# Optimization experiments

Hardware: AMD Instinct MI355X
Metric: run time of the kernel (lower is better)

## Reference

```python
import jax, jax.numpy as jnp
import numpy as np

B, T, D, F, E = 2, 2048, 1024, 4096, 8
TOP_K = 2


def setup_inputs() -> dict:
    key = jax.random.key(0)
    k0, k1, k2, k3 = jax.random.split(key, 4)
    x = jax.random.normal(k0, (B, T, D), dtype=jnp.float32)
    Wr = jax.random.normal(k1, (D, E), dtype=jnp.float32) * 0.02   # router (no bias)
    W1 = jax.random.normal(k2, (E, D, F), dtype=jnp.float32) * 0.02
    b1 = jnp.zeros((E, F), dtype=jnp.float32)
    W2 = jax.random.normal(k3, (E, F, D), dtype=jnp.float32) * 0.02
    b2 = jnp.zeros((E, D), dtype=jnp.float32)
    return {"x": x, "Wr": Wr, "W1": W1, "b1": b1, "W2": W2, "b2": b2}


def reference(x, Wr, W1, b1, W2, b2):
    # Router: softmax over experts, top-k select, renormalize selected probs.
    logits = jnp.einsum('btd,de->bte', x, Wr)                      # [B,T,E]
    probs = jax.nn.softmax(logits, axis=-1)
    top_v, top_i = jax.lax.top_k(probs, TOP_K)                     # [B,T,K]
    top_v = top_v / jnp.sum(top_v, axis=-1, keepdims=True)
    # Combine weights: scatter renormalized top-k probs back to expert slots.
    combine = jnp.sum(jax.nn.one_hot(top_i, E, dtype=x.dtype) * top_v[..., None], axis=-2)  # [B,T,E]
    # Expert FFNs (Linear -> exact GELU -> Linear); dropout inactive at eval.
    h = jax.nn.gelu(jnp.einsum('btd,edf->ebtf', x, W1) + b1[:, None, None, :],
                    approximate=False)                              # [E,B,T,F]
    y = jnp.einsum('ebtf,efd->ebtd', h, W2) + b2[:, None, None, :]  # [E,B,T,D]
    # Weighted sum over selected experts (combine is zero for unselected).
    out = jnp.einsum('ebtd,bte->btd', y, combine)
    return out
```

## Files before the change

### kernel.cpp

```cpp
#include <hip/hip_runtime.h>
#include <hip/hip_bf16.h>
#include <math.h>

#define B_  2
#define T_  2048
#define D_  1024
#define F_  4096
#define E_  8
#define NTOK 4096
#define TOPK 2
#define NROW 8192

typedef unsigned short bf16_t;
typedef float f32x4 __attribute__((ext_vector_type(4)));
typedef int   i32x4 __attribute__((ext_vector_type(4)));
typedef __bf16 bf16x8 __attribute__((ext_vector_type(8)));

#define OFF_CNT   0
#define OFF_BASE  32
#define OFF_TIDX  64
#define OFF_TW    32832
#define OFF_LIST  65600
#define OFF_WGT   196672
#define OFF_H_OLD 327744
#define WS_OLD    (OFF_H_OLD + (size_t)NROW * F_ * 2)
#define OFF_SLOT  327744
#define OFF_XB    (1u << 20)
#define OFF_W1T   (OFF_XB  + (size_t)NTOK * D_ * 2)
#define OFF_W2T   (OFF_W1T + (size_t)E_ * F_ * D_ * 2)
#define OFF_HN    (OFF_W2T + (size_t)E_ * D_ * F_ * 2)
#define OFF_Y     (OFF_HN  + (size_t)NROW * F_ * 2)
#define WS_MFMA   (OFF_Y + (size_t)NROW * D_ * 4)
#define WS_MFMA2  (OFF_Y + 2 * (size_t)NROW * D_ * 4)

__device__ __forceinline__ float gelu_exact(float v) {
    return 0.5f * v * (1.0f + erff(v * 0.70710678118654752440f));
}

__device__ __forceinline__ unsigned short f2bf_rne(float f) {
    union { float f; unsigned int u; } v; v.f = f;
    unsigned int r = (v.u + 0x7fffu + ((v.u >> 16) & 1u)) >> 16;
    return (unsigned short)r;
}

__device__ __forceinline__ float bf2f(unsigned int u) {
    union { unsigned int i; float f; } v; v.i = u << 16; return v.f;
}

__device__ __forceinline__ void gld16(const void* g, void* l) {
    __builtin_amdgcn_global_load_lds(
        (const __attribute__((address_space(1))) unsigned int*)g,
        (__attribute__((address_space(3))) unsigned int*)l, 16, 0, 0);
}

__device__ __forceinline__ void mfma16(const i32x4& a, const i32x4& b, f32x4& c) {
    c = __builtin_amdgcn_mfma_f32_16x16x32_bf16(
        __builtin_bit_cast(bf16x8, a), __builtin_bit_cast(bf16x8, b), c, 0, 0, 0);
}

__global__ __launch_bounds__(64) void router_kernel(
    const float* __restrict__ x, const float* __restrict__ Wr,
    int* __restrict__ top_idx, float* __restrict__ top_w,
    int* __restrict__ cnt, int* __restrict__ list, float* __restrict__ wgt,
    int* __restrict__ slot, int mode)
{
    const int n = blockIdx.x;
    const int lane = threadIdx.x;
    const float* xr = x + (size_t)n * D_;

    float acc[E_];
#pragma unroll
    for (int e = 0; e < E_; ++e) acc[e] = 0.f;

    for (int d = lane; d < D_; d += 64) {
        const float xv = xr[d];
#pragma unroll
        for (int e = 0; e < E_; ++e)
            acc[e] += xv * Wr[d * E_ + e];
    }
#pragma unroll
    for (int e = 0; e < E_; ++e) {
        float v = acc[e];
#pragma unroll
        for (int off = 32; off > 0; off >>= 1)
            v += __shfl_down(v, off, 64);
        acc[e] = v;
    }
    if (lane == 0) {
        float m = acc[0];
#pragma unroll
        for (int e = 1; e < E_; ++e) m = fmaxf(m, acc[e]);
        float p[E_];
#pragma unroll
        for (int e = 0; e < E_; ++e) p[e] = __expf(acc[e] - m);
        int i0 = 0; float v0 = p[0];
#pragma unroll
        for (int e = 1; e < E_; ++e) if (p[e] > v0) { v0 = p[e]; i0 = e; }
        int i1 = (i0 == 0) ? 1 : 0; float v1 = p[i1];
#pragma unroll
        for (int e = 0; e < E_; ++e) {
            if (e == i0) continue;
            if (p[e] > v1) { v1 = p[e]; i1 = e; }
        }
        const float inv = 1.f / (v0 + v1);
        const float w0 = v0 * inv, w1 = v1 * inv;
        top_idx[n * TOPK + 0] = i0;
        top_idx[n * TOPK + 1] = i1;
        top_w[n * TOPK + 0] = w0;
        top_w[n * TOPK + 1] = w1;
        if (mode & 1) {
            int p0 = atomicAdd(&cnt[i0], 1);
            list[i0 * NTOK + p0] = n;  wgt[i0 * NTOK + p0] = w0;
            int p1 = atomicAdd(&cnt[i1], 1);
            list[i1 * NTOK + p1] = n;  wgt[i1 * NTOK + p1] = w1;
            if (mode & 2) {
                slot[n * TOPK + 0] = (i0 << 16) | p0;
                slot[n * TOPK + 1] = (i1 << 16) | p1;
            }
        }
    }
}

__global__ void prefix_kernel(const int* __restrict__ cnt, int* __restrict__ base)
{
    if (threadIdx.x == 0 && blockIdx.x == 0) {
        int s = 0;
#pragma unroll
        for (int e = 0; e < E_; ++e) { base[e] = s; s += cnt[e]; }
    }
}

__global__ __launch_bounds__(256) void convert_x_kernel(
    const float* __restrict__ x, bf16_t* __restrict__ xb)
{
    const int i = blockIdx.x * 256 + threadIdx.x;
    const float4 v = ((const float4*)x)[i];
    uint2 o;
    o.x = (unsigned int)f2bf_rne(v.x) | ((unsigned int)f2bf_rne(v.y) << 16);
    o.y = (unsigned int)f2bf_rne(v.z) | ((unsigned int)f2bf_rne(v.w) << 16);
    ((uint2*)xb)[i] = o;
}

__global__ __launch_bounds__(256) void transpose_kernel(
    const float* __restrict__ src, bf16_t* __restrict__ dst, int R, int C)
{
    __shared__ float tile[64][65];
    const int z  = blockIdx.z;
    const int r0 = blockIdx.y * 64;
    const int c0 = blockIdx.x * 64;
    const float* s = src + (size_t)z * R * C;
    bf16_t*      d = dst + (size_t)z * R * C;
#pragma unroll
    for (int i = 0; i < 4; ++i) {
        const int r  = i * 16 + (threadIdx.x >> 4);
        const int c4 = (threadIdx.x & 15) * 4;
        const float4 v = *(const float4*)(s + (size_t)(r0 + r) * C + c0 + c4);
        tile[r][c4]     = v.x;
        tile[r][c4 + 1] = v.y;
        tile[r][c4 + 2] = v.z;
        tile[r][c4 + 3] = v.w;
    }
    __syncthreads();
    const int rc = (threadIdx.x & 15) * 4;
    const int cc = threadIdx.x >> 4;
#pragma unroll
    for (int i = 0; i < 4; ++i) {
        const int c = i * 16 + cc;
        uint2 o;
        o.x = (unsigned int)f2bf_rne(tile[rc    ][c]) | ((unsigned int)f2bf_rne(tile[rc + 1][c]) << 16);
        o.y = (unsigned int)f2bf_rne(tile[rc + 2][c]) | ((unsigned int)f2bf_rne(tile[rc + 3][c]) << 16);
        *(uint2*)(d + (size_t)(c0 + c) * R + r0 + rc) = o;
    }
}

template<int G>
__global__ __launch_bounds__(512, 2) void mg8_kernel(
    const bf16_t* __restrict__ Amat, const bf16_t* __restrict__ Bmat,
    const float* __restrict__ bias,
    const int* __restrict__ cnt, const int* __restrict__ base,
    const int* __restrict__ list,
    bf16_t* __restrict__ Hout, float* __restrict__ Yout)
{
    __shared__ __align__(16) bf16_t sm[3 * 16384];

    const int e  = (G == 1) ? blockIdx.z : (blockIdx.z % E_);
    const int ce = cnt[e];
    const int m0 = blockIdx.y * 256;
    if (m0 >= ce) return;
    const int n0 = blockIdx.x * 256;
    const int be = base[e];

    const int Kfull = (G == 1) ? D_ : F_;
    int klen, kbase, slab;
    if (G == 1) { klen = D_; kbase = 0; slab = 0; }
    else {
        const int kslabs = gridDim.z / E_;
        slab  = blockIdx.z / E_;
        klen  = F_ / kslabs;
        kbase = slab * klen;
    }
    const int nk = klen / 32;

    const int tid  = threadIdx.x;
    const int lane = tid & 63, wave = tid >> 6;
    const int l16 = lane & 15, quad = lane >> 4;
    const int wm = wave >> 2, wn = wave & 3;

    const int srow = wave * 16 + (lane >> 2);
    const int sgc  = (lane & 3) ^ ((srow >> 1) & 3);
    int rA0 = m0 + srow;        if (rA0 >= ce) rA0 = ce - 1;
    int rA1 = m0 + srow + 128;  if (rA1 >= ce) rA1 = ce - 1;
    const bf16_t *gA0, *gA1;
    if (G == 1) {
        gA0 = Amat + (size_t)list[e * NTOK + rA0] * D_ + sgc * 8;
        gA1 = Amat + (size_t)list[e * NTOK + rA1] * D_ + sgc * 8;
    } else {
        gA0 = Amat + (size_t)(be + rA0) * F_ + kbase + sgc * 8;
        gA1 = Amat + (size_t)(be + rA1) * F_ + kbase + sgc * 8;
    }
    const bf16_t* Be  = Bmat + (size_t)e * F_ * D_;
    const bf16_t* gB0 = Be + (size_t)(n0 + srow) * Kfull + kbase + sgc * 8;
    const bf16_t* gB1 = Be + (size_t)(n0 + srow + 128) * Kfull + kbase + sgc * 8;

#define STG(bb, kk) do { \
        bf16_t* la = sm + (bb) * 16384 + wave * 512; \
        bf16_t* lb = la + 8192; \
        gld16(gA0 + (kk), la); \
        gld16(gA1 + (kk), la + 4096); \
        gld16(gB0 + (kk), lb); \
        gld16(gB1 + (kk), lb + 4096); } while (0)

    const int swz  = (quad ^ ((l16 >> 1) & 3)) * 8;
    const int aoff = (wm * 128 + l16) * 32 + swz;
    const int boff = 8192 + (wn * 64 + l16) * 32 + swz;

    f32x4 acc[8][4] = {};

    STG(0, 0);
    STG(1, 32);
    asm volatile("s_waitcnt vmcnt(4)" ::: "memory");
    __builtin_amdgcn_s_barrier();
    __builtin_amdgcn_sched_barrier(0);

    int rb = 0;
    for (int t = 0; t < nk; ++t) {
        if (t + 2 < nk) {
            int wb = rb + 2; if (wb >= 3) wb -= 3;
            STG(wb, (t + 2) * 32);
        }
        const bf16_t* bp = sm + rb * 16384;
        i32x4 af[8], bv[4];
#pragma unroll
        for (int m = 0; m < 8; ++m)
            af[m] = *(const i32x4*)(bp + aoff + m * 512);
#pragma unroll
        for (int n = 0; n < 4; ++n)
            bv[n] = *(const i32x4*)(bp + boff + n * 512);
        __builtin_amdgcn_s_setprio(1);
#pragma unroll
        for (int m = 0; m < 8; ++m)
#pragma unroll
            for (int n = 0; n < 4; ++n)
                mfma16(af[m], bv[n], acc[m][n]);
        __builtin_amdgcn_s_setprio(0);
        if (t + 1 < nk) {
            if (t + 2 < nk) asm volatile("s_waitcnt vmcnt(4)" ::: "memory");
            else            asm volatile("s_waitcnt vmcnt(0)" ::: "memory");
            __builtin_amdgcn_s_barrier();
            __builtin_amdgcn_sched_barrier(0);
        }
        rb = (rb == 2) ? 0 : rb + 1;
    }
#undef STG

    if (G == 1) {
        const float* b1e = bias + (size_t)e * F_;
#pragma unroll
        for (int n = 0; n < 4; ++n) {
            const int col = n0 + wn * 64 + n * 16 + l16;
            const float bb = b1e[col];
#pragma unroll
            for (int m = 0; m < 8; ++m) {
                const int pr = m0 + wm * 128 + m * 16 + quad * 4;
#pragma unroll
                for (int r = 0; r < 4; ++r) {
                    const int p = pr + r;
                    if (p < ce)
                        Hout[(size_t)(be + p) * F_ + col] =
                            f2bf_rne(gelu_exact(acc[m][n][r] + bb));
                }
            }
        }
    } else {
        float* Ys = Yout + (size_t)slab * NROW * D_;
        const float* b2e = bias + (size_t)e * D_;
#pragma unroll
        for (int n = 0; n < 4; ++n) {
            const int col = n0 + wn * 64 + n * 16 + l16;
            const float bb = (slab == 0) ? b2e[col] : 0.f;
#pragma unroll
            for (int m = 0; m < 8; ++m) {
                const int pr = m0 + wm * 128 + m * 16 + quad * 4;
#pragma unroll
                for (int r = 0; r < 4; ++r) {
                    const int p = pr + r;
                    if (p < ce)
                        Ys[(size_t)(be + p) * D_ + col] = acc[m][n][r] + bb;
                }
            }
        }
    }
}

__global__ __launch_bounds__(256) void combine_kernel(
    const float* __restrict__ Y, const int* __restrict__ slot,
    const float* __restrict__ tw, const int* __restrict__ base,
    float* __restrict__ out, int kslabs)
{
    const int n = blockIdx.x;
    const int t = threadIdx.x;
    const int s0 = slot[n * TOPK + 0], s1 = slot[n * TOPK + 1];
    const float w0 = tw[n * TOPK + 0], w1 = tw[n * TOPK + 1];
    const int r0 = base[s0 >> 16] + (s0 & 0xffff);
    const int r1 = base[s1 >> 16] + (s1 & 0xffff);
    float4 y0 = ((const float4*)(Y + (size_t)r0 * D_))[t];
    float4 y1 = ((const float4*)(Y + (size_t)r1 * D_))[t];
    if (kslabs == 2) {
        const float* Y1 = Y + (size_t)NROW * D_;
        const float4 a = ((const float4*)(Y1 + (size_t)r0 * D_))[t];
        const float4 b = ((const float4*)(Y1 + (size_t)r1 * D_))[t];
        y0.x += a.x; y0.y += a.y; y0.z += a.z; y0.w += a.w;
        y1.x += b.x; y1.y += b.y; y1.z += b.z; y1.w += b.w;
    }
    float4 o;
    o.x = w0 * y0.x + w1 * y1.x;
    o.y = w0 * y0.y + w1 * y1.y;
    o.z = w0 * y0.z + w1 * y1.z;
    o.w = w0 * y0.w + w1 * y1.w;
    ((float4*)(out + (size_t)n * D_))[t] = o;
}

#define BM 128
#define BN 128
#define BK 16

__global__ __launch_bounds__(256) void gemm1_kernel(
    const float* __restrict__ x, const float* __restrict__ W1,
    const float* __restrict__ b1,
    const int* __restrict__ cnt, const int* __restrict__ base,
    const int* __restrict__ list, bf16_t* __restrict__ H)
{
    __shared__ __align__(16) float Xs[BK][BM + 4];
    __shared__ __align__(16) float Ws[BK][BN + 4];

    const int e  = blockIdx.z;
    const int ce = cnt[e];
    const int m0 = blockIdx.y * BM;
    if (m0 >= ce) return;
    const int n0 = blockIdx.x * BN;
    const int be = base[e];
    const int t  = threadIdx.x;
    const int tx = t & 15, ty = t >> 4;

    const int xr_row = t >> 1;
    const int xr_c0  = (t & 1) * 8;
    const int p_x    = m0 + xr_row;
    const float* xrow = (p_x < ce) ? (x + (size_t)list[e * NTOK + p_x] * D_) : nullptr;
    const int wr_kk = t >> 4;
    const int wr_c0 = (t & 15) * 8;
    const float* W1e = W1 + (size_t)e * D_ * F_;

    float acc[8][8];
#pragma unroll
    for (int i = 0; i < 8; ++i)
#pragma unroll
        for (int j = 0; j < 8; ++j) acc[i][j] = 0.f;

    for (int k0 = 0; k0 < D_; k0 += BK) {
        float xv[8];
        if (xrow) {
            const float4 a = *(const float4*)(xrow + k0 + xr_c0);
            const float4 b = *(const float4*)(xrow + k0 + xr_c0 + 4);
            xv[0]=a.x; xv[1]=a.y; xv[2]=a.z; xv[3]=a.w;
            xv[4]=b.x; xv[5]=b.y; xv[6]=b.z; xv[7]=b.w;
        } else {
#pragma unroll
            for (int j = 0; j < 8; ++j) xv[j] = 0.f;
        }
#pragma unroll
        for (int j = 0; j < 8; ++j) Xs[xr_c0 + j][xr_row] = xv[j];
        {
            const float* wr = W1e + (size_t)(k0 + wr_kk) * F_ + (n0 + wr_c0);
            *(float4*)&Ws[wr_kk][wr_c0]     = *(const float4*)(wr);
            *(float4*)&Ws[wr_kk][wr_c0 + 4] = *(const float4*)(wr + 4);
        }
        __syncthreads();
#pragma unroll 4
        for (int kk = 0; kk < BK; ++kk) {
            float a[8], b[8];
            *(float4*)&a[0] = *(const float4*)&Xs[kk][ty * 8];
            *(float4*)&a[4] = *(const float4*)&Xs[kk][ty * 8 + 4];
            *(float4*)&b[0] = *(const float4*)&Ws[kk][tx * 8];
            *(float4*)&b[4] = *(const float4*)&Ws[kk][tx * 8 + 4];
#pragma unroll
            for (int i = 0; i < 8; ++i)
#pragma unroll
                for (int j = 0; j < 8; ++j)
                    acc[i][j] += a[i] * b[j];
        }
        __syncthreads();
    }

    const float* b1e = b1 + (size_t)e * F_;
    float bb[8];
#pragma unroll
    for (int j = 0; j < 8; ++j) bb[j] = b1e[n0 + tx * 8 + j];
#pragma unroll
    for (int i = 0; i < 8; ++i) {
        const int p = m0 + ty * 8 + i;
        if (p >= ce) continue;
        unsigned int pk[4];
#pragma unroll
        for (int jj = 0; jj < 4; ++jj) {
            const float g0 = gelu_exact(acc[i][2 * jj]     + bb[2 * jj]);
            const float g1 = gelu_exact(acc[i][2 * jj + 1] + bb[2 * jj + 1]);
            pk[jj] = (unsigned int)f2bf_rne(g0) | ((unsigned int)f2bf_rne(g1) << 16);
        }
        uint4 v; v.x = pk[0]; v.y = pk[1]; v.z = pk[2]; v.w = pk[3];
        *(uint4*)(H + (size_t)(be + p) * F_ + n0 + tx * 8) = v;
    }
}

__global__ __launch_bounds__(256) void gemm2_kernel(
    const bf16_t* __restrict__ H, const float* __restrict__ W2,
    const float* __restrict__ b2,
    const int* __restrict__ cnt, const int* __restrict__ base,
    const int* __restrict__ list, const float* __restrict__ wgt,
    float* __restrict__ out)
{
    __shared__ __align__(16) float Hs[BK][BM + 4];
    __shared__ __align__(16) float Ws[BK][BN + 4];

    const int e  = blockIdx.z;
    const int ce = cnt[e];
    const int m0 = blockIdx.y * BM;
    if (m0 >= ce) return;
    const int n0 = blockIdx.x * BN;
    const int be = base[e];
    const int t  = threadIdx.x;
    const int tx = t & 15, ty = t >> 4;

    const int hr_row = t >> 1;
    const int hr_c0  = (t & 1) * 8;
    const int p_h    = m0 + hr_row;
    const bf16_t* hrow = (p_h < ce) ? (H + (size_t)(be + p_h) * F_) : nullptr;
    const int wr_kk = t >> 4;
    const int wr_c0 = (t & 15) * 8;
    const float* W2e = W2 + (size_t)e * F_ * D_;

    float acc[8][8];
#pragma unroll
    for (int i = 0; i < 8; ++i)
#pragma unroll
        for (int j = 0; j < 8; ++j) acc[i][j] = 0.f;

    for (int k0 = 0; k0 < F_; k0 += BK) {
        float hv[8];
        if (hrow) {
            const uint4 u = *(const uint4*)(hrow + k0 + hr_c0);
            hv[0] = bf2f(u.x & 0xffffu); hv[1] = bf2f(u.x >> 16);
            hv[2] = bf2f(u.y & 0xffffu); hv[3] = bf2f(u.y >> 16);
            hv[4] = bf2f(u.z & 0xffffu); hv[5] = bf2f(u.z >> 16);
            hv[6] = bf2f(u.w & 0xffffu); hv[7] = bf2f(u.w >> 16);
        } else {
#pragma unroll
            for (int j = 0; j < 8; ++j) hv[j] = 0.f;
        }
#pragma unroll
        for (int j = 0; j < 8; ++j) Hs[hr_c0 + j][hr_row] = hv[j];
        {
            const float* wr = W2e + (size_t)(k0 + wr_kk) * D_ + (n0 + wr_c0);
            *(float4*)&Ws[wr_kk][wr_c0]     = *(const float4*)(wr);
            *(float4*)&Ws[wr_kk][wr_c0 + 4] = *(const float4*)(wr + 4);
        }
        __syncthreads();
#pragma unroll 4
        for (int kk = 0; kk < BK; ++kk) {
            float a[8], b[8];
            *(float4*)&a[0] = *(const float4*)&Hs[kk][ty * 8];
            *(float4*)&a[4] = *(const float4*)&Hs[kk][ty * 8 + 4];
            *(float4*)&b[0] = *(const float4*)&Ws[kk][tx * 8];
            *(float4*)&b[4] = *(const float4*)&Ws[kk][tx * 8 + 4];
#pragma unroll
            for (int i = 0; i < 8; ++i)
#pragma unroll
                for (int j = 0; j < 8; ++j)
                    acc[i][j] += a[i] * b[j];
        }
        __syncthreads();
    }

    const float* b2e = b2 + (size_t)e * D_;
    float bb[8];
#pragma unroll
    for (int j = 0; j < 8; ++j) bb[j] = b2e[n0 + tx * 8 + j];
#pragma unroll
    for (int i = 0; i < 8; ++i) {
        const int p = m0 + ty * 8 + i;
        if (p >= ce) continue;
        const int   n = list[e * NTOK + p];
        const float w = wgt[e * NTOK + p];
        float* op = out + (size_t)n * D_ + n0 + tx * 8;
#pragma unroll
        for (int j = 0; j < 8; ++j)
            atomicAdd(&op[j], w * (acc[i][j] + bb[j]));
    }
}

__global__ __launch_bounds__(256) void fallback_expert_kernel(
    const float* __restrict__ x,
    const float* __restrict__ W1, const float* __restrict__ b1,
    const float* __restrict__ W2, const float* __restrict__ b2,
    const int* __restrict__ top_idx, const float* __restrict__ top_w,
    float* __restrict__ out)
{
    __shared__ float x_lds[D_];
    __shared__ float h_lds[F_];

    const int n = blockIdx.x;
    const int t = threadIdx.x;

    ((float4*)x_lds)[t] = ((const float4*)(x + (size_t)n * D_))[t];
    __syncthreads();

    const int d0 = t * 4;
    float acc_out[4] = {0.f, 0.f, 0.f, 0.f};

    for (int k = 0; k < TOPK; ++k) {
        const int   e = top_idx[n * TOPK + k];
        const float w = top_w[n * TOPK + k];
        const float* W1e = W1 + (size_t)e * D_ * F_;
        const float* b1e = b1 + (size_t)e * F_;
#pragma unroll
        for (int tile = 0; tile < 2; ++tile) {
            const int base_f = tile * 2048 + t * 8;
            float a[8];
#pragma unroll
            for (int j = 0; j < 8; ++j) a[j] = b1e[base_f + j];
            const float4* wp = (const float4*)(W1e + base_f);
            for (int d = 0; d < D_; ++d) {
                const float4 w0 = wp[(size_t)d * (F_ / 4)];
                const float4 w1 = wp[(size_t)d * (F_ / 4) + 1];
                const float xv = x_lds[d];
                a[0] += xv * w0.x; a[1] += xv * w0.y;
                a[2] += xv * w0.z; a[3] += xv * w0.w;
                a[4] += xv * w1.x; a[5] += xv * w1.y;
                a[6] += xv * w1.z; a[7] += xv * w1.w;
            }
#pragma unroll
            for (int j = 0; j < 8; ++j)
                h_lds[base_f + j] = gelu_exact(a[j]);
        }
        __syncthreads();

        const float* W2e = W2 + (size_t)e * F_ * D_;
        const float* b2e = b2 + (size_t)e * D_;
        float y[4];
#pragma unroll
        for (int j = 0; j < 4; ++j) y[j] = b2e[d0 + j];
        const float4* wp2 = (const float4*)(W2e + d0);
        for (int f = 0; f < F_; ++f) {
            const float4 wv = wp2[(size_t)f * (D_ / 4)];
            const float hv = h_lds[f];
            y[0] += hv * wv.x; y[1] += hv * wv.y;
            y[2] += hv * wv.z; y[3] += hv * wv.w;
        }
#pragma unroll
        for (int j = 0; j < 4; ++j) acc_out[j] += w * y[j];
        __syncthreads();
    }

    float4 o; o.x = acc_out[0]; o.y = acc_out[1]; o.z = acc_out[2]; o.w = acc_out[3];
    *(float4*)(out + (size_t)n * D_ + d0) = o;
}

extern "C" void kernel_launch(void* const* d_in, const int* in_sizes, int n_in,
                              void* d_out, int out_size, void* d_ws, size_t ws_size,
                              hipStream_t stream) {
    const float* x  = (const float*)d_in[0];
    const float* Wr = (const float*)d_in[1];
    const float* W1 = (const float*)d_in[2];
    const float* b1 = (const float*)d_in[3];
    const float* W2 = (const float*)d_in[4];
    const float* b2 = (const float*)d_in[5];
    float* out = (float*)d_out;

    char* ws = (char*)d_ws;
    int*    cnt   = (int*)(ws + OFF_CNT);
    int*    basep = (int*)(ws + OFF_BASE);
    int*    tidx  = (int*)(ws + OFF_TIDX);
    float*  tw    = (float*)(ws + OFF_TW);
    int*    list  = (int*)(ws + OFF_LIST);
    float*  wgt   = (float*)(ws + OFF_WGT);

    if (ws_size >= WS_MFMA) {
        const int kslabs = (ws_size >= WS_MFMA2) ? 2 : 1;
        int*    slot = (int*)(ws + OFF_SLOT);
        bf16_t* Xb   = (bf16_t*)(ws + OFF_XB);
        bf16_t* W1T  = (bf16_t*)(ws + OFF_W1T);
        bf16_t* W2T  = (bf16_t*)(ws + OFF_W2T);
        bf16_t* H    = (bf16_t*)(ws + OFF_HN);
        float*  Y    = (float*)(ws + OFF_Y);

        hipMemsetAsync(cnt, 0, E_ * sizeof(int), stream);
        router_kernel<<<NTOK, 64, 0, stream>>>(x, Wr, tidx, tw, cnt, list, wgt, slot, 3);
        prefix_kernel<<<1, 64, 0, stream>>>(cnt, basep);
        convert_x_kernel<<<NTOK * D_ / 4 / 256, 256, 0, stream>>>(x, Xb);
        transpose_kernel<<<dim3(F_ / 64, D_ / 64, E_), 256, 0, stream>>>(W1, W1T, D_, F_);
        transpose_kernel<<<dim3(D_ / 64, F_ / 64, E_), 256, 0, stream>>>(W2, W2T, F_, D_);
        mg8_kernel<1><<<dim3(F_ / 256, NTOK / 256, E_), 512, 0, stream>>>(
            Xb, W1T, b1, cnt, basep, list, H, nullptr);
        mg8_kernel<2><<<dim3(D_ / 256, NTOK / 256, E_ * kslabs), 512, 0, stream>>>(
            H, W2T, b2, cnt, basep, nullptr, nullptr, Y);
        combine_kernel<<<NTOK, 256, 0, stream>>>(Y, slot, tw, basep, out, kslabs);
    } else if (ws_size >= WS_OLD) {
        bf16_t* H = (bf16_t*)(ws + OFF_H_OLD);
        hipMemsetAsync(cnt, 0, E_ * sizeof(int), stream);
        router_kernel<<<NTOK, 64, 0, stream>>>(x, Wr, tidx, tw, cnt, list, wgt, nullptr, 1);
        prefix_kernel<<<1, 64, 0, stream>>>(cnt, basep);
        hipMemsetAsync(out, 0, (size_t)NTOK * D_ * sizeof(float), stream);
        gemm1_kernel<<<dim3(F_ / BN, NTOK / BM, E_), 256, 0, stream>>>(
            x, W1, b1, cnt, basep, list, H);
        gemm2_kernel<<<dim3(D_ / BN, NTOK / BM, E_), 256, 0, stream>>>(
            H, W2, b2, cnt, basep, list, wgt, out);
    } else {
        router_kernel<<<NTOK, 64, 0, stream>>>(x, Wr, tidx, tw, cnt, list, wgt, nullptr, 0);
        fallback_expert_kernel<<<NTOK, 256, 0, stream>>>(
            x, W1, b1, W2, b2, tidx, tw, out);
    }
}
```

Baseline: 736.1 us.

## Switch grouped GEMM to BK=64 double-buffered LDS pipeline

Replaces the three-stage BK=32 LDS pipeline with a two-stage BK=64 double buffer. The swizzle changes to an 8-way XOR over 64-column rows, and each wave issues eight 16-byte global-to-LDS loads per stage. The aim is to halve the number of barriers and loop iterations per K. In exchange the prefetch distance drops from two stages to one. The kernel now waits at a full __syncthreads instead of a partial vmcnt wait, so memory latency may be less well hidden.

Measured after the change: 730.7 us. About the same (-0.7%).

```diff
diff --git a/kernel.cpp b/kernel.cpp
--- a/kernel.cpp
+++ b/kernel.cpp
@@ -181,7 +181,7 @@
     const int* __restrict__ list,
     bf16_t* __restrict__ Hout, float* __restrict__ Yout)
 {
-    __shared__ __align__(16) bf16_t sm[3 * 16384];
+    __shared__ __align__(16) bf16_t sm[2 * 32768];
 
     const int e  = (G == 1) ? blockIdx.z : (blockIdx.z % E_);
     const int ce = cnt[e];
@@ -199,77 +199,73 @@
         klen  = F_ / kslabs;
         kbase = slab * klen;
     }
-    const int nk = klen / 32;
+    const int nkt = klen / 64;
 
     const int tid  = threadIdx.x;
     const int lane = tid & 63, wave = tid >> 6;
     const int l16 = lane & 15, quad = lane >> 4;
     const int wm = wave >> 2, wn = wave & 3;
 
-    const int srow = wave * 16 + (lane >> 2);
-    const int sgc  = (lane & 3) ^ ((srow >> 1) & 3);
-    int rA0 = m0 + srow;        if (rA0 >= ce) rA0 = ce - 1;
-    int rA1 = m0 + srow + 128;  if (rA1 >= ce) rA1 = ce - 1;
-    const bf16_t *gA0, *gA1;
-    if (G == 1) {
-        gA0 = Amat + (size_t)list[e * NTOK + rA0] * D_ + sgc * 8;
-        gA1 = Amat + (size_t)list[e * NTOK + rA1] * D_ + sgc * 8;
-    } else {
-        gA0 = Amat + (size_t)(be + rA0) * F_ + kbase + sgc * 8;
-        gA1 = Amat + (size_t)(be + rA1) * F_ + kbase + sgc * 8;
-    }
-    const bf16_t* Be  = Bmat + (size_t)e * F_ * D_;
-    const bf16_t* gB0 = Be + (size_t)(n0 + srow) * Kfull + kbase + sgc * 8;
-    const bf16_t* gB1 = Be + (size_t)(n0 + srow + 128) * Kfull + kbase + sgc * 8;
-
-#define STG(bb, kk) do { \
-        bf16_t* la = sm + (bb) * 16384 + wave * 512; \
-        bf16_t* lb = la + 8192; \
-        gld16(gA0 + (kk), la); \
-        gld16(gA1 + (kk), la + 4096); \
-        gld16(gB0 + (kk), lb); \
-        gld16(gB1 + (kk), lb + 4096); } while (0)
-
-    const int swz  = (quad ^ ((l16 >> 1) & 3)) * 8;
-    const int aoff = (wm * 128 + l16) * 32 + swz;
-    const int boff = 8192 + (wn * 64 + l16) * 32 + swz;
+    const int srowl = lane >> 3;
+    const int sgc   = ((lane & 7) ^ srowl) * 8;
+
+    const bf16_t* gA[4];
+    const bf16_t* gB[4];
+    const bf16_t* Be = Bmat + (size_t)e * F_ * D_;
+#pragma unroll
+    for (int i = 0; i < 4; ++i) {
+        int ra = m0 + wave * 32 + i * 8 + srowl;
+        if (ra >= ce) ra = ce - 1;
+        if (G == 1) gA[i] = Amat + (size_t)list[e * NTOK + ra] * D_ + sgc;
+        else        gA[i] = Amat + (size_t)(be + ra) * F_ + kbase + sgc;
+        const int rb = n0 + wave * 32 + i * 8 + srowl;
+        gB[i] = Be + (size_t)rb * Kfull + kbase + sgc;
+    }
+
+#define STG(bb, koff) do { \
+        bf16_t* la = sm + (bb) * 32768 + wave * 2048; \
+        bf16_t* lb = la + 16384; \
+        gld16(gA[0] + (koff), la); \
+        gld16(gA[1] + (koff), la + 512); \
+        gld16(gA[2] + (koff), la + 1024); \
+        gld16(gA[3] + (koff), la + 1536); \
+        gld16(gB[0] + (koff), lb); \
+        gld16(gB[1] + (koff), lb + 512); \
+        gld16(gB[2] + (koff), lb + 1024); \
+        gld16(gB[3] + (koff), lb + 1536); } while (0)
+
+    const int swzk[2] = { (quad ^ (l16 & 7)) * 8, ((4 + quad) ^ (l16 & 7)) * 8 };
+    const int arow = (wm * 128 + l16) * 64;
+    const int brow = 16384 + (wn * 64 + l16) * 64;
 
     f32x4 acc[8][4] = {};
 
     STG(0, 0);
-    STG(1, 32);
-    asm volatile("s_waitcnt vmcnt(4)" ::: "memory");
-    __builtin_amdgcn_s_barrier();
-    __builtin_amdgcn_sched_barrier(0);
-
-    int rb = 0;
-    for (int t = 0; t < nk; ++t) {
-        if (t + 2 < nk) {
-            int wb = rb + 2; if (wb >= 3) wb -= 3;
-            STG(wb, (t + 2) * 32);
-        }
-        const bf16_t* bp = sm + rb * 16384;
-        i32x4 af[8], bv[4];
-#pragma unroll
-        for (int m = 0; m < 8; ++m)
-            af[m] = *(const i32x4*)(bp + aoff + m * 512);
-#pragma unroll
-        for (int n = 0; n < 4; ++n)
-            bv[n] = *(const i32x4*)(bp + boff + n * 512);
-        __builtin_amdgcn_s_setprio(1);
-#pragma unroll
-        for (int m = 0; m < 8; ++m)
+    __syncthreads();
+
+    int buf = 0;
+    for (int kt = 0; kt < nkt; ++kt) {
+        if (kt + 1 < nkt) STG(buf ^ 1, (kt + 1) * 64);
+        const bf16_t* bp = sm + buf * 32768;
+#pragma unroll
+        for (int kk = 0; kk < 2; ++kk) {
+            i32x4 af[8], bv[4];
+#pragma unroll
+            for (int m = 0; m < 8; ++m)
+                af[m] = *(const i32x4*)(bp + arow + m * 1024 + swzk[kk]);
 #pragma unroll
             for (int n = 0; n < 4; ++n)
-                mfma16(af[m], bv[n], acc[m][n]);
-        __builtin_amdgcn_s_setprio(0);
-        if (t + 1 < nk) {
-            if (t + 2 < nk) asm volatile("s_waitcnt vmcnt(4)" ::: "memory");
-            else            asm volatile("s_waitcnt vmcnt(0)" ::: "memory");
-            __builtin_amdgcn_s_barrier();
-            __builtin_amdgcn_sched_barrier(0);
-        }
-        rb = (rb == 2) ? 0 : rb + 1;
+                bv[n] = *(const i32x4*)(bp + brow + n * 1024 + swzk[kk]);
+            __builtin_amdgcn_s_setprio(1);
+#pragma unroll
+            for (int m = 0; m < 8; ++m)
+#pragma unroll
+                for (int n = 0; n < 4; ++n)
+                    mfma16(af[m], bv[n], acc[m][n]);
+            __builtin_amdgcn_s_setprio(0);
+        }
+        __syncthreads();
+        buf ^= 1;
     }
 #undef STG
 
```
